# Performance work log

Hardware: AMD Instinct MI355X
Metric: run time of the kernel (lower is better)

Reference implementation:

```python
import jax, jax.numpy as jnp
import numpy as np

D_MODEL = 2048
NUM_HEADS = 32
NUM_KV_HEADS = 8
D_K = D_MODEL // NUM_HEADS
BATCH = 2
SEQ = 2048


def setup_inputs() -> dict:
    key = jax.random.key(0)
    ks = jax.random.split(key, 9)
    s_in = 1.0 / np.sqrt(D_MODEL)
    kv_dim = NUM_KV_HEADS * D_K
    return {
        "x": jax.random.normal(ks[0], (BATCH, SEQ, D_MODEL), jnp.float32),
        "Wq": jax.random.uniform(ks[1], (D_MODEL, D_MODEL), jnp.float32, -s_in, s_in),
        "bq": jax.random.uniform(ks[2], (D_MODEL,), jnp.float32, -s_in, s_in),
        "Wk": jax.random.uniform(ks[3], (D_MODEL, kv_dim), jnp.float32, -s_in, s_in),
        "bk": jax.random.uniform(ks[4], (kv_dim,), jnp.float32, -s_in, s_in),
        "Wv": jax.random.uniform(ks[5], (D_MODEL, kv_dim), jnp.float32, -s_in, s_in),
        "bv": jax.random.uniform(ks[6], (kv_dim,), jnp.float32, -s_in, s_in),
        "Wo": jax.random.uniform(ks[7], (D_MODEL, D_MODEL), jnp.float32, -s_in, s_in),
        "bo": jax.random.uniform(ks[8], (D_MODEL,), jnp.float32, -s_in, s_in),
    }


def reference(x, Wq, bq, Wk, bk, Wv, bv, Wo, bo):
    b, s, _ = x.shape
    rep = NUM_HEADS // NUM_KV_HEADS
    # projections
    q = (x @ Wq + bq).reshape(b, s, NUM_HEADS, D_K).transpose(0, 2, 1, 3)      # [b,h,s,d]
    k = (x @ Wk + bk).reshape(b, s, NUM_KV_HEADS, D_K).transpose(0, 2, 1, 3)   # [b,g,s,d]
    v = (x @ Wv + bv).reshape(b, s, NUM_KV_HEADS, D_K).transpose(0, 2, 1, 3)
    # repeat_interleave over kv heads (head h uses kv head h // rep)
    k = jnp.repeat(k, rep, axis=1)  # [b,h,s,d]
    v = jnp.repeat(v, rep, axis=1)
    scale = 1.0 / np.sqrt(D_K).astype(np.float32)
    scores = jnp.einsum("bhqd,bhkd->bhqk", q, k) * scale
    probs = jax.nn.softmax(scores, axis=-1)
    ctx = jnp.einsum("bhqk,bhkd->bhqd", probs, v)        # [b,h,s,d]
    ctx = ctx.transpose(0, 2, 1, 3).reshape(b, s, D_MODEL)
    return ctx @ Wo + bo
```

## Files before the change

kernel.cpp:

```cpp
#include <hip/hip_runtime.h>
#include <hip/hip_bf16.h>
#include <cstdint>

#define D_MODEL 2048
#define NHEADS 32
#define NKV 8
#define DK 64
#define BATCH 2
#define SEQ 2048
#define M_TOT (BATCH * SEQ)
#define KV_DIM (NKV * DK)
#define QSCALE 0.18033688011112042f
#define MSUB 20.0f

typedef __attribute__((ext_vector_type(8))) short short8;
typedef __attribute__((ext_vector_type(4))) short short4_;
typedef __attribute__((ext_vector_type(2))) float f32x2;
typedef __attribute__((ext_vector_type(4))) float f32x4;
typedef __attribute__((ext_vector_type(16))) float f32x16;
typedef unsigned short u16;
typedef unsigned int u32;

__device__ __forceinline__ u16 f2bf(float f) {
  u32 u = __builtin_bit_cast(u32, f);
  u += 0x7fffu + ((u >> 16) & 1u);
  return (u16)(u >> 16);
}

__device__ __forceinline__ u32 cvtpk(float a, float b) {
  u32 r;
  asm("v_cvt_pk_bf16_f32 %0, %1, %2" : "=v"(r) : "v"(a), "v"(b));
  return r;
}

__device__ __forceinline__ float exp2v(float x) {
  float r;
  asm("v_exp_f32 %0, %1" : "=v"(r) : "v"(x));
  return r;
}

__device__ __forceinline__ f32x2 pkadd(f32x2 a, f32x2 b) {
  f32x2 r;
  asm("v_pk_add_f32 %0, %1, %2" : "=v"(r) : "v"(a), "v"(b));
  return r;
}

__device__ __forceinline__ void gld_lds16(const u16* g, u16* l) {
  __builtin_amdgcn_global_load_lds((__attribute__((address_space(1))) void*)g,
                                   (__attribute__((address_space(3))) void*)l,
                                   16, 0, 0);
}

__global__ void k_convert(const float* __restrict__ in, u16* __restrict__ out, int n4) {
  int i = blockIdx.x * blockDim.x + threadIdx.x;
  if (i >= n4) return;
  float4 v = reinterpret_cast<const float4*>(in)[i];
  uint2 o;
  o.x = (u32)f2bf(v.x) | ((u32)f2bf(v.y) << 16);
  o.y = (u32)f2bf(v.z) | ((u32)f2bf(v.w) << 16);
  reinterpret_cast<uint2*>(out)[i] = o;
}

__global__ void k_transpose(const float* __restrict__ W, u16* __restrict__ Wt,
                            int K, int N) {
  __shared__ float tile[32][33];
  int n0 = blockIdx.x * 32, k0 = blockIdx.y * 32;
  int tx = threadIdx.x, ty = threadIdx.y;
#pragma unroll
  for (int j = 0; j < 4; ++j)
    tile[ty + j * 8][tx] = W[(size_t)(k0 + ty + j * 8) * N + n0 + tx];
  __syncthreads();
#pragma unroll
  for (int j = 0; j < 4; ++j)
    Wt[(size_t)(n0 + ty + j * 8) * K + k0 + tx] = f2bf(tile[tx][ty + j * 8]);
}

template <int MODE, int NBX, int NWG>
__global__ __launch_bounds__(256, 4) void k_gemm128(
    const u16* __restrict__ A, const u16* __restrict__ Bt,
    const float* __restrict__ b0, const float* __restrict__ b1,
    const float* __restrict__ b2,
    u16* __restrict__ O0, u16* __restrict__ O1, u16* __restrict__ O2,
    float* __restrict__ Of) {
  __shared__ u16 Alds[2][128 * 32];
  __shared__ u16 Blds[2][128 * 32];
  const int tid = threadIdx.x;
  const int lane = tid & 63;
  const int wid = tid >> 6;
  const int wr = wid >> 1, wc = wid & 1;
  const int l15 = lane & 15, lg = lane >> 4;
  const int bid = blockIdx.x;
  const int swz = (bid & 7) * (NWG / 8) + (bid >> 3);
  const int by = swz / NBX, bx = swz % NBX;
  const int row0 = by * 128, col0 = bx * 128;

  const u16* pa0 = A  + (size_t)(row0 + (tid >> 2)) * D_MODEL + (tid & 3) * 8;
  const u16* pa1 = pa0 + (size_t)64 * D_MODEL;
  const u16* pb0 = Bt + (size_t)(col0 + (tid >> 2)) * D_MODEL + (tid & 3) * 8;
  const u16* pb1 = pb0 + (size_t)64 * D_MODEL;

  f32x4 acc[4][4];
#pragma unroll
  for (int m = 0; m < 4; ++m)
#pragma unroll
    for (int n = 0; n < 4; ++n) acc[m][n] = (f32x4){0.f, 0.f, 0.f, 0.f};

#define GSTAGE(CUR, KOFF) do {                                                 \
  gld_lds16(pa0 + (KOFF), &Alds[CUR][tid * 8]);                                \
  gld_lds16(pa1 + (KOFF), &Alds[CUR][(tid + 256) * 8]);                        \
  gld_lds16(pb0 + (KOFF), &Blds[CUR][tid * 8]);                                \
  gld_lds16(pb1 + (KOFF), &Blds[CUR][(tid + 256) * 8]);                        \
} while (0)

#define GCOMPUTE(CUR) do {                                                     \
  short8 af_[4], bf_[4];                                                       \
  _Pragma("unroll")                                                            \
  for (int m = 0; m < 4; ++m)                                                  \
    af_[m] = *(const short8*)(&Alds[CUR][(wr * 64 + m * 16 + l15) * 32 + lg * 8]); \
  _Pragma("unroll")                                                            \
  for (int n = 0; n < 4; ++n)                                                  \
    bf_[n] = *(const short8*)(&Blds[CUR][(wc * 64 + n * 16 + l15) * 32 + lg * 8]); \
  _Pragma("unroll")                                                            \
  for (int m = 0; m < 4; ++m)                                                  \
    _Pragma("unroll")                                                          \
    for (int n = 0; n < 4; ++n)                                                \
      acc[m][n] = __builtin_amdgcn_mfma_f32_16x16x32_bf16(af_[m], bf_[n], acc[m][n], 0, 0, 0); \
} while (0)

  GSTAGE(0, 0);
  for (int kt = 0; kt < 64; kt += 2) {
    __syncthreads();
    if (kt + 1 < 64) GSTAGE(1, (kt + 1) * 32);
    GCOMPUTE(0);
    __syncthreads();
    if (kt + 2 < 64) GSTAGE(0, (kt + 2) * 32);
    GCOMPUTE(1);
  }
#undef GSTAGE
#undef GCOMPUTE

  if (MODE == 1) {
#pragma unroll
    for (int m = 0; m < 4; ++m)
#pragma unroll
      for (int n = 0; n < 4; ++n) {
        int col = col0 + wc * 64 + n * 16 + l15;
        float bb = b0[col];
#pragma unroll
        for (int j = 0; j < 4; ++j) {
          int row = row0 + wr * 64 + m * 16 + lg * 4 + j;
          Of[(size_t)row * D_MODEL + col] = acc[m][n][j] + bb;
        }
      }
  } else if (col0 < 2048) {
#pragma unroll
    for (int m = 0; m < 4; ++m)
#pragma unroll
      for (int n = 0; n < 4; ++n) {
        int col = col0 + wc * 64 + n * 16 + l15;
        float bb = b0[col];
#pragma unroll
        for (int j = 0; j < 4; ++j) {
          int row = row0 + wr * 64 + m * 16 + lg * 4 + j;
          O0[(size_t)row * D_MODEL + col] = f2bf((acc[m][n][j] + bb) * QSCALE);
        }
      }
  } else if (col0 < 2560) {
#pragma unroll
    for (int m = 0; m < 4; ++m)
#pragma unroll
      for (int n = 0; n < 4; ++n) {
        int ck = col0 - 2048 + wc * 64 + n * 16 + l15;
        float bb = b1[ck];
#pragma unroll
        for (int j = 0; j < 4; ++j) {
          int row = row0 + wr * 64 + m * 16 + lg * 4 + j;
          O1[(size_t)row * KV_DIM + ck] = f2bf(acc[m][n][j] + bb);
        }
      }
  } else {
#pragma unroll
    for (int m = 0; m < 4; ++m)
#pragma unroll
      for (int n = 0; n < 4; ++n) {
        int dv = col0 - 2560 + wc * 64 + n * 16 + l15;
        float bb = b2[dv];
        int rowb = row0 + wr * 64 + m * 16 + lg * 4;
        short4_ w;
#pragma unroll
        for (int j = 0; j < 4; ++j) w[j] = (short)f2bf(acc[m][n][j] + bb);
        *(short4_*)(O2 + (size_t)dv * M_TOT + rowb) = w;
      }
  }
}

__global__ __launch_bounds__(512) void k_attn(
    const u16* __restrict__ Qb, const u16* __restrict__ Kb,
    const u16* __restrict__ Vt, u16* __restrict__ Ctx) {
  __shared__ u16 smem[6 * 4096];
  const int tid = threadIdx.x;
  const int lane = tid & 63;
  const int wid = tid >> 6;
  const int l31 = lane & 31;
  const int hi = lane >> 5;
  const int b = blockIdx.z, h = blockIdx.y, g = h >> 2;
  const int qrow = blockIdx.x * 256 + wid * 32 + l31;
  const size_t tok = (size_t)b * SEQ + qrow;

  short8 qf[4];
  const u16* qp = Qb + tok * D_MODEL + h * DK + hi * 8;
#pragma unroll
  for (int d = 0; d < 4; ++d) qf[d] = *(const short8*)(qp + d * 16);

  f32x16 oacc0, oacc1;
#pragma unroll
  for (int i = 0; i < 16; ++i) { oacc0[i] = 0.f; oacc1[i] = 0.f; }
  float lrun = 0.f;

  char* sm = (char*)smem;
  const u16* Ksrc = Kb + (size_t)b * SEQ * KV_DIM + g * DK;
  const u16* Vsrc = Vt + (size_t)g * DK * M_TOT + b * SEQ;

#define STAGE(CUR, KV0) do {                                                   \
  int r_ = tid >> 3, c_ = tid & 7, cg_ = c_ ^ (r_ & 7);                        \
  gld_lds16(Ksrc + (size_t)((KV0) + r_) * KV_DIM + cg_ * 8,                    \
            smem + (CUR) * 4096 + tid * 8);                                    \
  gld_lds16(Vsrc + (size_t)r_ * M_TOT + (KV0) + cg_ * 8,                       \
            smem + 12288 + (CUR) * 4096 + tid * 8);                            \
} while (0)

  STAGE(0, 0);
  STAGE(1, 64);

  int cur = 0;
  const int r0 = l31, r1 = 32 + l31;

#pragma unroll 1
  for (int t = 0; t < 32; ++t) {
    if (t < 31) {
      asm volatile("s_waitcnt vmcnt(2)" ::: "memory");
    } else {
      asm volatile("s_waitcnt vmcnt(0)" ::: "memory");
    }
    __builtin_amdgcn_s_barrier();
    __builtin_amdgcn_sched_barrier(0);

    if (t + 2 < 32) {
      int nx = cur + 2; if (nx >= 3) nx -= 3;
      STAGE(nx, (t + 2) * 64);
    }

    const char* kbase = sm + cur * 8192;
    const char* vbase = sm + 24576 + cur * 8192;

    f32x16 sacc0, sacc1;
#pragma unroll
    for (int i = 0; i < 16; ++i) { sacc0[i] = 0.f; sacc1[i] = 0.f; }
    __builtin_amdgcn_s_setprio(1);
#pragma unroll
    for (int d = 0; d < 4; ++d) {
      short8 k0 = *(const short8*)(kbase + r0 * 128 + (((d * 2 + hi) ^ (r0 & 7)) * 16));
      short8 k1 = *(const short8*)(kbase + r1 * 128 + (((d * 2 + hi) ^ (r1 & 7)) * 16));
      sacc0 = __builtin_amdgcn_mfma_f32_32x32x16_bf16(k0, qf[d], sacc0, 0, 0, 0);
      sacc1 = __builtin_amdgcn_mfma_f32_32x32x16_bf16(k1, qf[d], sacc1, 0, 0, 0);
    }
    __builtin_amdgcn_s_setprio(0);

    float pe0[16], pe1[16];
    f32x2 sA = (f32x2){0.f, 0.f}, sB = (f32x2){0.f, 0.f};
    const f32x2 negM = (f32x2){-MSUB, -MSUB};
#pragma unroll
    for (int i = 0; i < 8; ++i) {
      f32x2 a0 = pkadd((f32x2){sacc0[2 * i], sacc0[2 * i + 1]}, negM);
      f32x2 a1 = pkadd((f32x2){sacc1[2 * i], sacc1[2 * i + 1]}, negM);
      pe0[2 * i] = exp2v(a0[0]);
      pe0[2 * i + 1] = exp2v(a0[1]);
      pe1[2 * i] = exp2v(a1[0]);
      pe1[2 * i + 1] = exp2v(a1[1]);
      sA = pkadd(sA, (f32x2){pe0[2 * i], pe0[2 * i + 1]});
      sB = pkadd(sB, (f32x2){pe1[2 * i], pe1[2 * i + 1]});
    }
    float s32 = (sA[0] + sA[1]) + (sB[0] + sB[1]);
    {
      u32 xs = __builtin_bit_cast(u32, s32), ys = xs;
      asm volatile("v_permlane32_swap_b32 %0, %1" : "+v"(xs), "+v"(ys));
      lrun += __builtin_bit_cast(float, xs) + __builtin_bit_cast(float, ys);
    }

#define PV_STEP(PE, RB, KB) do {                                               \
  u32 w0_ = cvtpk(PE[(RB) + 0], PE[(RB) + 1]);                                 \
  u32 w1_ = cvtpk(PE[(RB) + 2], PE[(RB) + 3]);                                 \
  u32 w2_ = cvtpk(PE[(RB) + 4], PE[(RB) + 5]);                                 \
  u32 w3_ = cvtpk(PE[(RB) + 6], PE[(RB) + 7]);                                 \
  asm volatile("v_permlane32_swap_b32 %0, %1" : "+v"(w0_), "+v"(w2_));         \
  asm volatile("v_permlane32_swap_b32 %0, %1" : "+v"(w1_), "+v"(w3_));         \
  union { u32 w[4]; short8 s8; } uu_;                                          \
  uu_.w[0] = w0_; uu_.w[1] = w1_; uu_.w[2] = w2_; uu_.w[3] = w3_;              \
  short8 pf_ = uu_.s8;                                                         \
  short8 vf0_ = *(const short8*)(vbase + r0 * 128 + ((((KB) * 2 + hi) ^ (r0 & 7)) * 16)); \
  short8 vf1_ = *(const short8*)(vbase + r1 * 128 + ((((KB) * 2 + hi) ^ (r1 & 7)) * 16)); \
  __builtin_amdgcn_s_setprio(1);                                               \
  oacc0 = __builtin_amdgcn_mfma_f32_32x32x16_bf16(vf0_, pf_, oacc0, 0, 0, 0);  \
  oacc1 = __builtin_amdgcn_mfma_f32_32x32x16_bf16(vf1_, pf_, oacc1, 0, 0, 0);  \
  __builtin_amdgcn_s_setprio(0);                                               \
} while (0)

    PV_STEP(pe0, 0, 0);
    PV_STEP(pe0, 8, 1);
    PV_STEP(pe1, 0, 2);
    PV_STEP(pe1, 8, 3);
#undef PV_STEP

    ++cur; if (cur == 3) cur = 0;
  }

  float rl = 1.0f / lrun;
  u16* cp = Ctx + tok * D_MODEL + h * DK;
#pragma unroll
  for (int db = 0; db < 2; ++db) {
    const f32x16& oa = db ? oacc1 : oacc0;
#pragma unroll
    for (int quad = 0; quad < 4; ++quad) {
      int dbase = db * 32 + 8 * quad + 4 * hi;
      short4_ w;
#pragma unroll
      for (int j = 0; j < 4; ++j) w[j] = (short)f2bf(oa[quad * 4 + j] * rl);
      *(short4_*)(cp + dbase) = w;
    }
  }
#undef STAGE
}

extern "C" void kernel_launch(void* const* d_in, const int* in_sizes, int n_in,
                              void* d_out, int out_size, void* d_ws, size_t ws_size,
                              hipStream_t stream) {
  const float* x  = (const float*)d_in[0];
  const float* Wq = (const float*)d_in[1];
  const float* bq = (const float*)d_in[2];
  const float* Wk = (const float*)d_in[3];
  const float* bk = (const float*)d_in[4];
  const float* Wv = (const float*)d_in[5];
  const float* bv = (const float*)d_in[6];
  const float* Wo = (const float*)d_in[7];
  const float* bo = (const float*)d_in[8];
  float* out = (float*)d_out;

  char* ws = (char*)d_ws;
  u16* xb    = (u16*)(ws);
  u16* Wqkvt = (u16*)(ws + 16777216);
  u16* Wot   = (u16*)(ws + 29360128);
  u16* Qb    = (u16*)(ws + 37748736);
  u16* Kb    = (u16*)(ws + 54525952);
  u16* Vtr   = (u16*)(ws + 58720256);
  u16* Ctx   = (u16*)(ws + 62914560);

  int n4 = M_TOT * D_MODEL / 4;
  k_convert<<<(n4 + 255) / 256, 256, 0, stream>>>(x, xb, n4);
  k_transpose<<<dim3(64, 64), dim3(32, 8), 0, stream>>>(Wq, Wqkvt, D_MODEL, D_MODEL);
  k_transpose<<<dim3(16, 64), dim3(32, 8), 0, stream>>>(Wk, Wqkvt + (size_t)2048 * D_MODEL, D_MODEL, KV_DIM);
  k_transpose<<<dim3(16, 64), dim3(32, 8), 0, stream>>>(Wv, Wqkvt + (size_t)2560 * D_MODEL, D_MODEL, KV_DIM);
  k_transpose<<<dim3(64, 64), dim3(32, 8), 0, stream>>>(Wo, Wot, D_MODEL, D_MODEL);

  k_gemm128<0, 24, 768><<<768, 256, 0, stream>>>(xb, Wqkvt, bq, bk, bv, Qb, Kb, Vtr, nullptr);

  k_attn<<<dim3(SEQ / 256, NHEADS, BATCH), 512, 0, stream>>>(Qb, Kb, Vtr, Ctx);

  k_gemm128<1, 16, 512><<<512, 256, 0, stream>>>(Ctx, Wot, bo, nullptr, nullptr,
                                                 nullptr, nullptr, nullptr, out);
}
```

Baseline: 220.1 us.

## Triple-buffer GEMM LDS pipeline with explicit vmcnt waits and MFMA priority

Moves the 128x128 GEMM main loop from double to triple LDS buffering with a prefetch distance of two k-tiles. Each k-step now has one s_waitcnt vmcnt plus a single barrier instead of two __syncthreads. MFMA sections are wrapped in s_setprio so compute-issuing waves get scheduling priority. The cost is 50% more shared memory per block, which may lower how many blocks fit on a CU under the 4-block launch bound.

```diff
diff --git a/kernel.cpp b/kernel.cpp
--- a/kernel.cpp
+++ b/kernel.cpp
@@ -82,8 +82,8 @@
     const float* __restrict__ b2,
     u16* __restrict__ O0, u16* __restrict__ O1, u16* __restrict__ O2,
     float* __restrict__ Of) {
-  __shared__ u16 Alds[2][128 * 32];
-  __shared__ u16 Blds[2][128 * 32];
+  __shared__ u16 Alds[3][128 * 32];
+  __shared__ u16 Blds[3][128 * 32];
   const int tid = threadIdx.x;
   const int lane = tid & 63;
   const int wid = tid >> 6;
@@ -105,11 +105,11 @@
 #pragma unroll
     for (int n = 0; n < 4; ++n) acc[m][n] = (f32x4){0.f, 0.f, 0.f, 0.f};
 
-#define GSTAGE(CUR, KOFF) do {                                                 \
-  gld_lds16(pa0 + (KOFF), &Alds[CUR][tid * 8]);                                \
-  gld_lds16(pa1 + (KOFF), &Alds[CUR][(tid + 256) * 8]);                        \
-  gld_lds16(pb0 + (KOFF), &Blds[CUR][tid * 8]);                                \
-  gld_lds16(pb1 + (KOFF), &Blds[CUR][(tid + 256) * 8]);                        \
+#define GSTAGE(NB, KOFF) do {                                                  \
+  gld_lds16(pa0 + (KOFF), &Alds[NB][tid * 8]);                                 \
+  gld_lds16(pa1 + (KOFF), &Alds[NB][(tid + 256) * 8]);                         \
+  gld_lds16(pb0 + (KOFF), &Blds[NB][tid * 8]);                                 \
+  gld_lds16(pb1 + (KOFF), &Blds[NB][(tid + 256) * 8]);                         \
 } while (0)
 
 #define GCOMPUTE(CUR) do {                                                     \
@@ -120,22 +120,33 @@
   _Pragma("unroll")                                                            \
   for (int n = 0; n < 4; ++n)                                                  \
     bf_[n] = *(const short8*)(&Blds[CUR][(wc * 64 + n * 16 + l15) * 32 + lg * 8]); \
+  __builtin_amdgcn_s_setprio(1);                                               \
   _Pragma("unroll")                                                            \
   for (int m = 0; m < 4; ++m)                                                  \
     _Pragma("unroll")                                                          \
     for (int n = 0; n < 4; ++n)                                                \
       acc[m][n] = __builtin_amdgcn_mfma_f32_16x16x32_bf16(af_[m], bf_[n], acc[m][n], 0, 0, 0); \
+  __builtin_amdgcn_s_setprio(0);                                               \
+} while (0)
+
+#define ITER(KT, B, VM) do {                                                   \
+  asm volatile("s_waitcnt vmcnt(" VM ")" ::: "memory");                        \
+  __builtin_amdgcn_s_barrier();                                                \
+  __builtin_amdgcn_sched_barrier(0);                                           \
+  if ((KT) + 2 < 64) GSTAGE((B + 2) % 3, ((KT) + 2) * 32);                     \
+  GCOMPUTE(B);                                                                 \
 } while (0)
 
   GSTAGE(0, 0);
-  for (int kt = 0; kt < 64; kt += 2) {
-    __syncthreads();
-    if (kt + 1 < 64) GSTAGE(1, (kt + 1) * 32);
-    GCOMPUTE(0);
-    __syncthreads();
-    if (kt + 2 < 64) GSTAGE(0, (kt + 2) * 32);
-    GCOMPUTE(1);
+  GSTAGE(1, 32);
+#pragma unroll 1
+  for (int kt = 0; kt < 63; kt += 3) {
+    ITER(kt, 0, "4");
+    ITER(kt + 1, 1, "4");
+    ITER(kt + 2, 2, "4");
   }
+  ITER(63, 0, "0");
+#undef ITER
 #undef GSTAGE
 #undef GCOMPUTE
 
```

Result: slower. 246.5 us (+12.0%).
